# Optimization experiments

Hardware: AMD Instinct MI355X
Metric: run time of the kernel (lower is better)

## Reference

```python
import jax, jax.numpy as jnp
import numpy as np

N_SRC = 1_000_000   # rows in the flattened layer_values store
D = 64              # feature dim
E = 4_000_000       # total gathered inputs across all neurons (ragged fan-in)
N_SEG = 250_000     # number of output neurons (segments)


def setup_inputs() -> dict:
    key = jax.random.key(0)
    k1, k2, k3 = jax.random.split(key, 3)
    layer_values = jax.random.normal(k1, (N_SRC, D), dtype=jnp.float32)
    gather_idx = jax.random.randint(k2, (E,), 0, N_SRC, dtype=jnp.int64) if jax.config.jax_enable_x64 else jax.random.randint(k2, (E,), 0, N_SRC, dtype=jnp.int32)
    segment_ids = jnp.sort(jax.random.randint(k3, (E,), 0, N_SEG, dtype=jnp.int32))
    return {
        "layer_values": layer_values,
        "gather_idx": gather_idx,
        "segment_ids": segment_ids,
        "n_segments": N_SEG,
    }


def reference(layer_values, gather_idx, segment_ids, n_segments):
    # 1) gather module: pick the input value row for every (neuron, input) pair
    gathered = jnp.take(layer_values, gather_idx, axis=0)          # [E, D]
    # 2) ragged segment-mean (equivalent to split/pad_sequence/sum/divide branch,
    #    and to the reshape+mean branch when all fan-ins match)
    sums = jax.ops.segment_sum(gathered, segment_ids, num_segments=n_segments)  # [N_SEG, D]
    counts = jax.ops.segment_sum(
        jnp.ones((gathered.shape[0],), dtype=gathered.dtype),
        segment_ids, num_segments=n_segments)                       # [N_SEG]
    y = sums / jnp.maximum(counts, 1.0)[:, None]                     # segment mean
    return y
```

## Files before the change

kernel.cpp:

```cpp
#include <hip/hip_runtime.h>

#define D 64

typedef float vfloat4 __attribute__((ext_vector_type(4)));

__global__ __launch_bounds__(256) void seg_starts_kernel(
    const int* __restrict__ sids, int E, int nseg, int* __restrict__ starts) {
    int e = blockIdx.x * blockDim.x + threadIdx.x;
    if (e >= E) return;
    int cur = __builtin_nontemporal_load(&sids[e]);
    int prev = (e == 0) ? -1 : __builtin_nontemporal_load(&sids[e - 1]);
    for (int s = prev + 1; s <= cur; ++s) starts[s] = e;
    if (e == E - 1) {
        for (int s = cur + 1; s <= nseg; ++s) starts[s] = E;
    }
}

__global__ __launch_bounds__(256) void seg_mean_kernel(
    const float* __restrict__ vals, const int* __restrict__ gidx,
    const int* __restrict__ sids, const int* __restrict__ starts,
    float* __restrict__ out, int E, int nseg) {
    int lane = threadIdx.x & 63;
    int seg = blockIdx.x * (blockDim.x >> 6) + (threadIdx.x >> 6);
    if (seg >= nseg) return;
    int sub = lane >> 4;
    int c16 = (lane & 15) << 4;

    int start, end;
    if (starts) {
        start = starts[seg];
        end   = starts[seg + 1];
    } else {
        int lo = 0, hi = E;
        while (lo < hi) { int m = (lo + hi) >> 1; if (sids[m] < seg) lo = m + 1; else hi = m; }
        start = lo;
        int lo2 = start, hi2 = E;
        while (lo2 < hi2) { int m = (lo2 + hi2) >> 1; if (sids[m] < seg + 1) lo2 = m + 1; else hi2 = m; }
        end = lo2;
    }
    int cnt = end - start;

    const char* vbase = (const char*)vals;
    vfloat4 a0 = {0,0,0,0}, a1 = {0,0,0,0}, a2 = {0,0,0,0}, a3 = {0,0,0,0};

    for (int base = start; base < end; base += 64) {
        int n = end - base;
        if (n > 64) n = 64;
        int l = (lane < n) ? lane : (n - 1);
        int my = __builtin_nontemporal_load(&gidx[base + l]);

        int j = 0;
        for (; j + 16 <= n; j += 16) {
            int i0 = __shfl(my, j +  0 + sub, 64);
            int i1 = __shfl(my, j +  4 + sub, 64);
            int i2 = __shfl(my, j +  8 + sub, 64);
            int i3 = __shfl(my, j + 12 + sub, 64);
            vfloat4 v0 = *(const vfloat4*)(vbase + (((unsigned)i0 << 8) | c16));
            vfloat4 v1 = *(const vfloat4*)(vbase + (((unsigned)i1 << 8) | c16));
            vfloat4 v2 = *(const vfloat4*)(vbase + (((unsigned)i2 << 8) | c16));
            vfloat4 v3 = *(const vfloat4*)(vbase + (((unsigned)i3 << 8) | c16));
            a0 += v0; a1 += v1; a2 += v2; a3 += v3;
        }
        if (j < n) {
            int e0 = j + sub, e1 = j + 4 + sub, e2 = j + 8 + sub, e3 = j + 12 + sub;
            int s0 = (e0 < n) ? e0 : (n - 1);
            int s1 = (e1 < n) ? e1 : (n - 1);
            int s2 = (e2 < n) ? e2 : (n - 1);
            int s3 = (e3 < n) ? e3 : (n - 1);
            int i0 = __shfl(my, s0, 64);
            int i1 = __shfl(my, s1, 64);
            int i2 = __shfl(my, s2, 64);
            int i3 = __shfl(my, s3, 64);
            vfloat4 v0 = *(const vfloat4*)(vbase + (((unsigned)i0 << 8) | c16));
            vfloat4 v1 = *(const vfloat4*)(vbase + (((unsigned)i1 << 8) | c16));
            vfloat4 v2 = *(const vfloat4*)(vbase + (((unsigned)i2 << 8) | c16));
            vfloat4 v3 = *(const vfloat4*)(vbase + (((unsigned)i3 << 8) | c16));
            a0 += v0 * ((e0 < n) ? 1.0f : 0.0f);
            a1 += v1 * ((e1 < n) ? 1.0f : 0.0f);
            a2 += v2 * ((e2 < n) ? 1.0f : 0.0f);
            a3 += v3 * ((e3 < n) ? 1.0f : 0.0f);
        }
    }

    a0 += a1; a2 += a3; a0 += a2;
    a0.x += __shfl_xor(a0.x, 16, 64); a0.y += __shfl_xor(a0.y, 16, 64);
    a0.z += __shfl_xor(a0.z, 16, 64); a0.w += __shfl_xor(a0.w, 16, 64);
    a0.x += __shfl_xor(a0.x, 32, 64); a0.y += __shfl_xor(a0.y, 32, 64);
    a0.z += __shfl_xor(a0.z, 32, 64); a0.w += __shfl_xor(a0.w, 32, 64);

    float inv = 1.0f / (float)((cnt > 0) ? cnt : 1);
    if (sub == 0) {
        vfloat4 r = a0 * inv;
        __builtin_nontemporal_store(r, (vfloat4*)((char*)out + (((unsigned)seg << 8) | c16)));
    }
}

extern "C" void kernel_launch(void* const* d_in, const int* in_sizes, int n_in,
                              void* d_out, int out_size, void* d_ws, size_t ws_size,
                              hipStream_t stream) {
    const float* vals = (const float*)d_in[0];
    const int*   gidx = (const int*)d_in[1];
    const int*   sids = (const int*)d_in[2];
    float*       out  = (float*)d_out;

    int E = in_sizes[1];
    int nseg = out_size / D;

    int* starts = nullptr;
    size_t need = (size_t)(nseg + 1) * sizeof(int);
    if (ws_size >= need) {
        starts = (int*)d_ws;
        int blocks = (E + 255) / 256;
        seg_starts_kernel<<<blocks, 256, 0, stream>>>(sids, E, nseg, starts);
    }

    const int waves_per_block = 4;
    int blocks2 = (nseg + waves_per_block - 1) / waves_per_block;
    seg_mean_kernel<<<blocks2, waves_per_block * 64, 0, stream>>>(
        vals, gidx, sids, starts, out, E, nseg);
}
```

Measured before the change: 462.0 us.

## Process two adjacent segments per wavefront with a merged gather loop

Each wavefront now handles two consecutive segments and walks their combined input range in 64-wide chunks. Each gathered row is routed to one of two accumulators based on its position relative to the segment boundary. With an average fan-in of about 16, this fills the 16-row load groups better and cuts partial tail iterations and per-segment setup. In exchange there are half as many wavefronts, more select and multiply arithmetic per row, and a second cross-lane reduction.

```diff
diff --git a/kernel.cpp b/kernel.cpp
--- a/kernel.cpp
+++ b/kernel.cpp
@@ -21,77 +21,88 @@
     const int* __restrict__ sids, const int* __restrict__ starts,
     float* __restrict__ out, int E, int nseg) {
     int lane = threadIdx.x & 63;
-    int seg = blockIdx.x * (blockDim.x >> 6) + (threadIdx.x >> 6);
-    if (seg >= nseg) return;
+    int wid = blockIdx.x * (blockDim.x >> 6) + (threadIdx.x >> 6);
+    int s0 = wid << 1;
+    if (s0 >= nseg) return;
+    int s0u = __builtin_amdgcn_readfirstlane(s0);
+    int sTop = s0u + 2; if (sTop > nseg) sTop = nseg;
+
+    int b0, b1, b2;
+    if (starts) {
+        b0 = starts[s0u];
+        b1 = starts[s0u + 1];
+        b2 = starts[sTop];
+    } else {
+        int lo = 0, hi = E;
+        while (lo < hi) { int m = (lo + hi) >> 1; if (sids[m] < s0u) lo = m + 1; else hi = m; }
+        b0 = lo;
+        lo = b0; hi = E;
+        while (lo < hi) { int m = (lo + hi) >> 1; if (sids[m] < s0u + 1) lo = m + 1; else hi = m; }
+        b1 = lo;
+        lo = b1; hi = E;
+        while (lo < hi) { int m = (lo + hi) >> 1; if (sids[m] < sTop) lo = m + 1; else hi = m; }
+        b2 = lo;
+    }
+
     int sub = lane >> 4;
     int c16 = (lane & 15) << 4;
 
-    int start, end;
-    if (starts) {
-        start = starts[seg];
-        end   = starts[seg + 1];
-    } else {
-        int lo = 0, hi = E;
-        while (lo < hi) { int m = (lo + hi) >> 1; if (sids[m] < seg) lo = m + 1; else hi = m; }
-        start = lo;
-        int lo2 = start, hi2 = E;
-        while (lo2 < hi2) { int m = (lo2 + hi2) >> 1; if (sids[m] < seg + 1) lo2 = m + 1; else hi2 = m; }
-        end = lo2;
-    }
-    int cnt = end - start;
+    const char* vbase = (const char*)vals;
+    vfloat4 acc0 = {0,0,0,0}, acc1 = {0,0,0,0};
 
-    const char* vbase = (const char*)vals;
-    vfloat4 a0 = {0,0,0,0}, a1 = {0,0,0,0}, a2 = {0,0,0,0}, a3 = {0,0,0,0};
+    for (int cb = b0; cb < b2; cb += 64) {
+        int n = b2 - cb;
+        if (n > 64) n = 64;
+        int t1 = b1 - cb;
+        int l = (lane < n) ? lane : (n - 1);
+        int my = __builtin_nontemporal_load(&gidx[cb + l]);
 
-    for (int base = start; base < end; base += 64) {
-        int n = end - base;
-        if (n > 64) n = 64;
-        int l = (lane < n) ? lane : (n - 1);
-        int my = __builtin_nontemporal_load(&gidx[base + l]);
-
-        int j = 0;
-        for (; j + 16 <= n; j += 16) {
-            int i0 = __shfl(my, j +  0 + sub, 64);
-            int i1 = __shfl(my, j +  4 + sub, 64);
-            int i2 = __shfl(my, j +  8 + sub, 64);
-            int i3 = __shfl(my, j + 12 + sub, 64);
-            vfloat4 v0 = *(const vfloat4*)(vbase + (((unsigned)i0 << 8) | c16));
-            vfloat4 v1 = *(const vfloat4*)(vbase + (((unsigned)i1 << 8) | c16));
-            vfloat4 v2 = *(const vfloat4*)(vbase + (((unsigned)i2 << 8) | c16));
-            vfloat4 v3 = *(const vfloat4*)(vbase + (((unsigned)i3 << 8) | c16));
-            a0 += v0; a1 += v1; a2 += v2; a3 += v3;
-        }
-        if (j < n) {
-            int e0 = j + sub, e1 = j + 4 + sub, e2 = j + 8 + sub, e3 = j + 12 + sub;
-            int s0 = (e0 < n) ? e0 : (n - 1);
-            int s1 = (e1 < n) ? e1 : (n - 1);
-            int s2 = (e2 < n) ? e2 : (n - 1);
-            int s3 = (e3 < n) ? e3 : (n - 1);
-            int i0 = __shfl(my, s0, 64);
-            int i1 = __shfl(my, s1, 64);
-            int i2 = __shfl(my, s2, 64);
-            int i3 = __shfl(my, s3, 64);
-            vfloat4 v0 = *(const vfloat4*)(vbase + (((unsigned)i0 << 8) | c16));
-            vfloat4 v1 = *(const vfloat4*)(vbase + (((unsigned)i1 << 8) | c16));
-            vfloat4 v2 = *(const vfloat4*)(vbase + (((unsigned)i2 << 8) | c16));
-            vfloat4 v3 = *(const vfloat4*)(vbase + (((unsigned)i3 << 8) | c16));
-            a0 += v0 * ((e0 < n) ? 1.0f : 0.0f);
-            a1 += v1 * ((e1 < n) ? 1.0f : 0.0f);
-            a2 += v2 * ((e2 < n) ? 1.0f : 0.0f);
-            a3 += v3 * ((e3 < n) ? 1.0f : 0.0f);
+        #pragma unroll
+        for (int j = 0; j < 64; j += 16) {
+            if (j < n) {
+                int e0 = j + sub, e1 = j + 4 + sub, e2 = j + 8 + sub, e3 = j + 12 + sub;
+                int q0 = (e0 < n) ? e0 : (n - 1);
+                int q1 = (e1 < n) ? e1 : (n - 1);
+                int q2 = (e2 < n) ? e2 : (n - 1);
+                int q3 = (e3 < n) ? e3 : (n - 1);
+                int i0 = __shfl(my, q0, 64);
+                int i1 = __shfl(my, q1, 64);
+                int i2 = __shfl(my, q2, 64);
+                int i3 = __shfl(my, q3, 64);
+                vfloat4 v0 = *(const vfloat4*)(vbase + (((unsigned)i0 << 8) | c16));
+                vfloat4 v1 = *(const vfloat4*)(vbase + (((unsigned)i1 << 8) | c16));
+                vfloat4 v2 = *(const vfloat4*)(vbase + (((unsigned)i2 << 8) | c16));
+                vfloat4 v3 = *(const vfloat4*)(vbase + (((unsigned)i3 << 8) | c16));
+                float w0 = (e0 < n) ? 1.0f : 0.0f, z0 = (e0 < n && e0 >= t1) ? 1.0f : 0.0f;
+                float w1 = (e1 < n) ? 1.0f : 0.0f, z1 = (e1 < n && e1 >= t1) ? 1.0f : 0.0f;
+                float w2 = (e2 < n) ? 1.0f : 0.0f, z2 = (e2 < n && e2 >= t1) ? 1.0f : 0.0f;
+                float w3 = (e3 < n) ? 1.0f : 0.0f, z3 = (e3 < n && e3 >= t1) ? 1.0f : 0.0f;
+                acc0 += v0 * (w0 - z0); acc1 += v0 * z0;
+                acc0 += v1 * (w1 - z1); acc1 += v1 * z1;
+                acc0 += v2 * (w2 - z2); acc1 += v2 * z2;
+                acc0 += v3 * (w3 - z3); acc1 += v3 * z3;
+            }
         }
     }
 
-    a0 += a1; a2 += a3; a0 += a2;
-    a0.x += __shfl_xor(a0.x, 16, 64); a0.y += __shfl_xor(a0.y, 16, 64);
-    a0.z += __shfl_xor(a0.z, 16, 64); a0.w += __shfl_xor(a0.w, 16, 64);
-    a0.x += __shfl_xor(a0.x, 32, 64); a0.y += __shfl_xor(a0.y, 32, 64);
-    a0.z += __shfl_xor(a0.z, 32, 64); a0.w += __shfl_xor(a0.w, 32, 64);
+    acc0.x += __shfl_xor(acc0.x, 16, 64); acc0.y += __shfl_xor(acc0.y, 16, 64);
+    acc0.z += __shfl_xor(acc0.z, 16, 64); acc0.w += __shfl_xor(acc0.w, 16, 64);
+    acc0.x += __shfl_xor(acc0.x, 32, 64); acc0.y += __shfl_xor(acc0.y, 32, 64);
+    acc0.z += __shfl_xor(acc0.z, 32, 64); acc0.w += __shfl_xor(acc0.w, 32, 64);
+    acc1.x += __shfl_xor(acc1.x, 16, 64); acc1.y += __shfl_xor(acc1.y, 16, 64);
+    acc1.z += __shfl_xor(acc1.z, 16, 64); acc1.w += __shfl_xor(acc1.w, 16, 64);
+    acc1.x += __shfl_xor(acc1.x, 32, 64); acc1.y += __shfl_xor(acc1.y, 32, 64);
+    acc1.z += __shfl_xor(acc1.z, 32, 64); acc1.w += __shfl_xor(acc1.w, 32, 64);
 
-    float inv = 1.0f / (float)((cnt > 0) ? cnt : 1);
+    int cnt0 = b1 - b0, cnt1 = b2 - b1;
     if (sub == 0) {
-        vfloat4 r = a0 * inv;
-        __builtin_nontemporal_store(r, (vfloat4*)((char*)out + (((unsigned)seg << 8) | c16)));
+        float inv = 1.0f / (float)((cnt0 > 0) ? cnt0 : 1);
+        vfloat4 r = acc0 * inv;
+        __builtin_nontemporal_store(r, (vfloat4*)((char*)out + (((unsigned)s0 << 8) | c16)));
+    } else if (sub == 1 && s0 + 1 < nseg) {
+        float inv = 1.0f / (float)((cnt1 > 0) ? cnt1 : 1);
+        vfloat4 r = acc1 * inv;
+        __builtin_nontemporal_store(r, (vfloat4*)((char*)out + (((unsigned)(s0 + 1) << 8) | c16)));
     }
 }
 
@@ -115,7 +126,8 @@
     }
 
     const int waves_per_block = 4;
-    int blocks2 = (nseg + waves_per_block - 1) / waves_per_block;
+    int waves = (nseg + 1) >> 1;
+    int blocks2 = (waves + waves_per_block - 1) / waves_per_block;
     seg_mean_kernel<<<blocks2, waves_per_block * 64, 0, stream>>>(
         vals, gidx, sids, starts, out, E, nseg);
 }
```

Result: no change. 462.6 us (+0.1%).

## Split segment-mean into two passes over halves of the source rows

Applied to the files above, without the earlier changes.

The gather-reduce now runs as two kernel launches, each taking contributions only from rows in one half of the value table. The first pass writes partial sums and the second adds its half and divides by the count. The aim is for each pass's working set (about 128 MB of source rows) to fit better in the last-level cache. The cost is reading indices twice, issuing masked loads that still fetch a dummy row for out-of-range entries, and an extra read and write of the output.

```diff
diff --git a/kernel.cpp b/kernel.cpp
--- a/kernel.cpp
+++ b/kernel.cpp
@@ -16,10 +16,11 @@
     }
 }
 
-__global__ __launch_bounds__(256) void seg_mean_kernel(
+template <int PHASE>
+__global__ __launch_bounds__(256) void seg_mean_phase_kernel(
     const float* __restrict__ vals, const int* __restrict__ gidx,
     const int* __restrict__ sids, const int* __restrict__ starts,
-    float* __restrict__ out, int E, int nseg) {
+    float* __restrict__ out, int E, int nseg, int rowLo, int rowHi) {
     int lane = threadIdx.x & 63;
     int seg = blockIdx.x * (blockDim.x >> 6) + (threadIdx.x >> 6);
     if (seg >= nseg) return;
@@ -41,6 +42,7 @@
     int cnt = end - start;
 
     const char* vbase = (const char*)vals;
+    unsigned span = (unsigned)(rowHi - rowLo);
     vfloat4 a0 = {0,0,0,0}, a1 = {0,0,0,0}, a2 = {0,0,0,0}, a3 = {0,0,0,0};
 
     for (int base = start; base < end; base += 64) {
@@ -55,11 +57,22 @@
             int i1 = __shfl(my, j +  4 + sub, 64);
             int i2 = __shfl(my, j +  8 + sub, 64);
             int i3 = __shfl(my, j + 12 + sub, 64);
-            vfloat4 v0 = *(const vfloat4*)(vbase + (((unsigned)i0 << 8) | c16));
-            vfloat4 v1 = *(const vfloat4*)(vbase + (((unsigned)i1 << 8) | c16));
-            vfloat4 v2 = *(const vfloat4*)(vbase + (((unsigned)i2 << 8) | c16));
-            vfloat4 v3 = *(const vfloat4*)(vbase + (((unsigned)i3 << 8) | c16));
-            a0 += v0; a1 += v1; a2 += v2; a3 += v3;
+            bool h0 = (unsigned)(i0 - rowLo) < span;
+            bool h1 = (unsigned)(i1 - rowLo) < span;
+            bool h2 = (unsigned)(i2 - rowLo) < span;
+            bool h3 = (unsigned)(i3 - rowLo) < span;
+            int p0 = h0 ? i0 : rowLo;
+            int p1 = h1 ? i1 : rowLo;
+            int p2 = h2 ? i2 : rowLo;
+            int p3 = h3 ? i3 : rowLo;
+            vfloat4 v0 = *(const vfloat4*)(vbase + (((unsigned)p0 << 8) | c16));
+            vfloat4 v1 = *(const vfloat4*)(vbase + (((unsigned)p1 << 8) | c16));
+            vfloat4 v2 = *(const vfloat4*)(vbase + (((unsigned)p2 << 8) | c16));
+            vfloat4 v3 = *(const vfloat4*)(vbase + (((unsigned)p3 << 8) | c16));
+            a0 += v0 * (h0 ? 1.0f : 0.0f);
+            a1 += v1 * (h1 ? 1.0f : 0.0f);
+            a2 += v2 * (h2 ? 1.0f : 0.0f);
+            a3 += v3 * (h3 ? 1.0f : 0.0f);
         }
         if (j < n) {
             int e0 = j + sub, e1 = j + 4 + sub, e2 = j + 8 + sub, e3 = j + 12 + sub;
@@ -71,14 +84,22 @@
             int i1 = __shfl(my, s1, 64);
             int i2 = __shfl(my, s2, 64);
             int i3 = __shfl(my, s3, 64);
-            vfloat4 v0 = *(const vfloat4*)(vbase + (((unsigned)i0 << 8) | c16));
-            vfloat4 v1 = *(const vfloat4*)(vbase + (((unsigned)i1 << 8) | c16));
-            vfloat4 v2 = *(const vfloat4*)(vbase + (((unsigned)i2 << 8) | c16));
-            vfloat4 v3 = *(const vfloat4*)(vbase + (((unsigned)i3 << 8) | c16));
-            a0 += v0 * ((e0 < n) ? 1.0f : 0.0f);
-            a1 += v1 * ((e1 < n) ? 1.0f : 0.0f);
-            a2 += v2 * ((e2 < n) ? 1.0f : 0.0f);
-            a3 += v3 * ((e3 < n) ? 1.0f : 0.0f);
+            bool h0 = ((unsigned)(i0 - rowLo) < span) && (e0 < n);
+            bool h1 = ((unsigned)(i1 - rowLo) < span) && (e1 < n);
+            bool h2 = ((unsigned)(i2 - rowLo) < span) && (e2 < n);
+            bool h3 = ((unsigned)(i3 - rowLo) < span) && (e3 < n);
+            int p0 = h0 ? i0 : rowLo;
+            int p1 = h1 ? i1 : rowLo;
+            int p2 = h2 ? i2 : rowLo;
+            int p3 = h3 ? i3 : rowLo;
+            vfloat4 v0 = *(const vfloat4*)(vbase + (((unsigned)p0 << 8) | c16));
+            vfloat4 v1 = *(const vfloat4*)(vbase + (((unsigned)p1 << 8) | c16));
+            vfloat4 v2 = *(const vfloat4*)(vbase + (((unsigned)p2 << 8) | c16));
+            vfloat4 v3 = *(const vfloat4*)(vbase + (((unsigned)p3 << 8) | c16));
+            a0 += v0 * (h0 ? 1.0f : 0.0f);
+            a1 += v1 * (h1 ? 1.0f : 0.0f);
+            a2 += v2 * (h2 ? 1.0f : 0.0f);
+            a3 += v3 * (h3 ? 1.0f : 0.0f);
         }
     }
 
@@ -88,10 +109,16 @@
     a0.x += __shfl_xor(a0.x, 32, 64); a0.y += __shfl_xor(a0.y, 32, 64);
     a0.z += __shfl_xor(a0.z, 32, 64); a0.w += __shfl_xor(a0.w, 32, 64);
 
-    float inv = 1.0f / (float)((cnt > 0) ? cnt : 1);
     if (sub == 0) {
-        vfloat4 r = a0 * inv;
-        __builtin_nontemporal_store(r, (vfloat4*)((char*)out + (((unsigned)seg << 8) | c16)));
+        char* op = (char*)out + (((unsigned)seg << 8) | c16);
+        if (PHASE == 0) {
+            *(vfloat4*)op = a0;
+        } else {
+            vfloat4 prev = *(const vfloat4*)op;
+            float inv = 1.0f / (float)((cnt > 0) ? cnt : 1);
+            vfloat4 r = (prev + a0) * inv;
+            __builtin_nontemporal_store(r, (vfloat4*)op);
+        }
     }
 }
 
@@ -105,6 +132,9 @@
 
     int E = in_sizes[1];
     int nseg = out_size / D;
+    int nsrc_rows = in_sizes[0] / D;
+    int Nh = nsrc_rows >> 1;
+    if (Nh < 1) Nh = 1;
 
     int* starts = nullptr;
     size_t need = (size_t)(nseg + 1) * sizeof(int);
@@ -116,6 +146,8 @@
 
     const int waves_per_block = 4;
     int blocks2 = (nseg + waves_per_block - 1) / waves_per_block;
-    seg_mean_kernel<<<blocks2, waves_per_block * 64, 0, stream>>>(
-        vals, gidx, sids, starts, out, E, nseg);
+    seg_mean_phase_kernel<0><<<blocks2, waves_per_block * 64, 0, stream>>>(
+        vals, gidx, sids, starts, out, E, nseg, 0, Nh);
+    seg_mean_phase_kernel<1><<<blocks2, waves_per_block * 64, 0, stream>>>(
+        vals, gidx, sids, starts, out, E, nseg, Nh, 0x7fffffff);
 }
```

Result: slower. 551.7 us (+19.4%).
